# Kernel tuning notes

Hardware: AMD Instinct MI355X
Metric: run time of the kernel (lower is better)

Reference implementation:

```python
import jax, jax.numpy as jnp
import numpy as np

BATCH = 4096
DIM = 512
TEMP = 0.5

def setup_inputs() -> dict:
    key = jax.random.key(0)
    k1, k2 = jax.random.split(key)
    emb_i = jax.random.normal(k1, (BATCH, DIM), dtype=jnp.float32)
    emb_j = jax.random.normal(k2, (BATCH, DIM), dtype=jnp.float32)
    return {"emb_i": emb_i, "emb_j": emb_j}

def reference(emb_i, emb_j):
    n = emb_i.shape[0]
    # L2-normalize once (torch F.normalize uses eps=1e-12 clamp on norm)
    z_i = emb_i / jnp.maximum(jnp.linalg.norm(emb_i, axis=1, keepdims=True), 1e-12)
    z_j = emb_j / jnp.maximum(jnp.linalg.norm(emb_j, axis=1, keepdims=True), 1e-12)
    z = jnp.concatenate([z_i, z_j], axis=0)            # [2N, D]
    sim = jnp.einsum('nd,md->nm', z, z)                # cosine sim, single GEMM
    # positives: diag(sim, +N) and diag(sim, -N) == rowwise dot(z_i, z_j)
    pos_ij = jnp.sum(z_i * z_j, axis=1)                # [N]
    positives = jnp.concatenate([pos_ij, pos_ij], 0)   # [2N]
    exp_sim = jnp.exp(sim / TEMP)
    mask = 1.0 - jnp.eye(2 * n, dtype=sim.dtype)
    denom = jnp.sum(mask * exp_sim, axis=1)            # [2N]
    loss_partial = -(positives / TEMP - jnp.log(denom))
    return jnp.sum(loss_partial) / (2 * n)
```

## Files before the change

### kernel.cpp

```cpp
#include <hip/hip_runtime.h>
#include <hip/hip_bf16.h>

#define N_ROWS 4096
#define DIM 512
#define TWO_N 8192
#define NTILE 64
#define NTRI  (NTILE * (NTILE + 1) / 2)

typedef __bf16 bf16x8 __attribute__((ext_vector_type(8)));
typedef float  f32x4  __attribute__((ext_vector_type(4)));

__device__ inline unsigned short f2bf(float f) {
    unsigned int u = __float_as_uint(f);
    u += 0x7fffu + ((u >> 16) & 1u);
    return (unsigned short)(u >> 16);
}

__device__ inline void g2l16(const void* g, void* l) {
    __builtin_amdgcn_global_load_lds(
        (const __attribute__((address_space(1))) void*)g,
        (__attribute__((address_space(3))) void*)l,
        16, 0, 0);
}

__global__ void normalize_kernel(const float* __restrict__ ei,
                                 const float* __restrict__ ej,
                                 unsigned short* __restrict__ zb,
                                 float* __restrict__ pos,
                                 float* __restrict__ denom,
                                 float* __restrict__ out) {
    int r = blockIdx.x;
    int t = threadIdx.x;
    const float2 vi = ((const float2*)(ei + (size_t)r * DIM))[t];
    const float2 vj = ((const float2*)(ej + (size_t)r * DIM))[t];
    float si  = vi.x * vi.x + vi.y * vi.y;
    float sj  = vj.x * vj.x + vj.y * vj.y;
    float sij = vi.x * vj.x + vi.y * vj.y;

    for (int o = 32; o; o >>= 1) {
        si  += __shfl_down(si, o);
        sj  += __shfl_down(sj, o);
        sij += __shfl_down(sij, o);
    }
    __shared__ float red[3][4];
    int wave = t >> 6, lane = t & 63;
    if (lane == 0) { red[0][wave] = si; red[1][wave] = sj; red[2][wave] = sij; }
    __syncthreads();
    si  = red[0][0] + red[0][1] + red[0][2] + red[0][3];
    sj  = red[1][0] + red[1][1] + red[1][2] + red[1][3];
    sij = red[2][0] + red[2][1] + red[2][2] + red[2][3];

    float rni = 1.0f / fmaxf(sqrtf(si), 1e-12f);
    float rnj = 1.0f / fmaxf(sqrtf(sj), 1e-12f);
    if (t == 0) {
        pos[r] = sij * rni * rnj;
        denom[r] = 0.0f;
        denom[r + N_ROWS] = 0.0f;
        if (r == 0) out[0] = 0.0f;
    }
    ushort2 zi2 = make_ushort2(f2bf(vi.x * rni), f2bf(vi.y * rni));
    ushort2 zj2 = make_ushort2(f2bf(vj.x * rnj), f2bf(vj.y * rnj));
    ((ushort2*)(zb + (size_t)r * DIM))[t] = zi2;
    ((ushort2*)(zb + (size_t)(r + N_ROWS) * DIM))[t] = zj2;
}

__global__ __launch_bounds__(256, 4) void gemm_exp_kernel(
        const unsigned short* __restrict__ zb,
        float* __restrict__ denom) {
    const int t = blockIdx.x;
    int by = (int)(0.5f * (2.0f * NTILE + 1.0f -
              sqrtf((2.0f * NTILE + 1.0f) * (2.0f * NTILE + 1.0f) - 8.0f * t)));
    while ((by + 1) * NTILE - ((by + 1) * by) / 2 <= t) ++by;
    while (by * NTILE - (by * (by - 1)) / 2 > t) --by;
    const int bx = by + (t - (by * NTILE - (by * (by - 1)) / 2));

    const int rb = by * 128;
    const int cb = bx * 128;
    const bool diag = (rb == cb);

    const int tid  = threadIdx.x;
    const int wave = tid >> 6;
    const int lane = tid & 63;
    const int quad = lane >> 4;
    const int m    = lane & 15;
    const int wm   = (wave >> 1) * 64;
    const int wn   = (wave & 1) * 64;

    __shared__ __align__(16) unsigned short As[128 * 64];
    __shared__ __align__(16) unsigned short Bs[128 * 64];

    f32x4 acc[4][4];
    #pragma unroll
    for (int i = 0; i < 4; ++i)
        #pragma unroll
        for (int j = 0; j < 4; ++j)
            #pragma unroll
            for (int r = 0; r < 4; ++r) acc[i][j][r] = 0.0f;

    const int srow8 = lane >> 3;
    const int sk    = (((lane & 7) ^ srow8) * 8);

    for (int it = 0; it < DIM / 64; ++it) {
        if (it) __syncthreads();
        const int k0 = it * 64;
        #pragma unroll
        for (int cc = 0; cc < 4; ++cc) {
            int c   = 4 * wave + cc;
            int row = c * 8 + srow8;
            const unsigned short* ga = zb + (size_t)(rb + row) * DIM + k0 + sk;
            const unsigned short* gb = zb + (size_t)(cb + row) * DIM + k0 + sk;
            g2l16(ga, As + c * 512);
            g2l16(gb, Bs + c * 512);
        }
        __syncthreads();

        #pragma unroll
        for (int h = 0; h < 2; ++h) {
            bf16x8 af[4], bfr[4];
            const int sl = ((((h << 2) | quad) ^ (m & 7)) * 8);
            #pragma unroll
            for (int i = 0; i < 4; ++i)
                af[i] = *(const bf16x8*)(As + (wm + i * 16 + m) * 64 + sl);
            #pragma unroll
            for (int j = 0; j < 4; ++j)
                bfr[j] = *(const bf16x8*)(Bs + (wn + j * 16 + m) * 64 + sl);

            #pragma unroll
            for (int i = 0; i < 4; ++i)
                #pragma unroll
                for (int j = 0; j < 4; ++j)
                    acc[i][j] = __builtin_amdgcn_mfma_f32_16x16x32_bf16(
                        af[i], bfr[j], acc[i][j], 0, 0, 0);
        }
    }

    __syncthreads();

    float* rs = (float*)As;
    float* cs = rs + 128;
    if (tid < 128) { rs[tid] = 0.0f; cs[tid] = 0.0f; }
    __syncthreads();

    float colsum[4] = {0.0f, 0.0f, 0.0f, 0.0f};
    #pragma unroll
    for (int i = 0; i < 4; ++i) {
        #pragma unroll
        for (int r = 0; r < 4; ++r) {
            int lrow = wm + i * 16 + quad * 4 + r;
            int grow = rb + lrow;
            float s = 0.0f;
            #pragma unroll
            for (int j = 0; j < 4; ++j) {
                int gcol = cb + wn + j * 16 + m;
                float v  = __expf(2.0f * acc[i][j][r]);
                v = (grow == gcol) ? 0.0f : v;
                s += v;
                colsum[j] += v;
            }
            s += __shfl_xor(s, 1);
            s += __shfl_xor(s, 2);
            s += __shfl_xor(s, 4);
            s += __shfl_xor(s, 8);
            if (m == 0) atomicAdd(&rs[lrow], s);
        }
    }
    if (!diag) {
        #pragma unroll
        for (int j = 0; j < 4; ++j) {
            float s = colsum[j];
            s += __shfl_xor(s, 16);
            s += __shfl_xor(s, 32);
            if (quad == 0) atomicAdd(&cs[wn + j * 16 + m], s);
        }
    }
    __syncthreads();
    if (tid < 128) {
        atomicAdd(&denom[rb + tid], rs[tid]);
        if (!diag) atomicAdd(&denom[cb + tid], cs[tid]);
    }
}

__global__ void loss_kernel(const float* __restrict__ pos,
                            const float* __restrict__ denom,
                            float* __restrict__ out) {
    int r = blockIdx.x * 256 + threadIdx.x;
    float s = __logf(denom[r]) - 2.0f * pos[r & (N_ROWS - 1)];
    for (int o = 32; o; o >>= 1) s += __shfl_down(s, o);
    __shared__ float red[4];
    int t = threadIdx.x;
    if ((t & 63) == 0) red[t >> 6] = s;
    __syncthreads();
    if (t == 0)
        atomicAdd(out, (red[0] + red[1] + red[2] + red[3]) / (float)TWO_N);
}

extern "C" void kernel_launch(void* const* d_in, const int* in_sizes, int n_in,
                              void* d_out, int out_size, void* d_ws, size_t ws_size,
                              hipStream_t stream) {
    const float* ei = (const float*)d_in[0];
    const float* ej = (const float*)d_in[1];

    unsigned short* zb  = (unsigned short*)d_ws;
    float* pos   = (float*)((char*)d_ws + (size_t)TWO_N * DIM * sizeof(unsigned short));
    float* denom = pos + N_ROWS;
    float* out   = (float*)d_out;

    normalize_kernel<<<N_ROWS, 256, 0, stream>>>(ei, ej, zb, pos, denom, out);
    gemm_exp_kernel<<<NTRI, 256, 0, stream>>>(zb, denom);
    loss_kernel<<<TWO_N / 256, 256, 0, stream>>>(pos, denom, out);
}
```

Baseline: 122.1 us.

## Use 256x256 tiles with 8 waves and double-buffered LDS prefetch

```diff
diff --git a/kernel.cpp b/kernel.cpp
--- a/kernel.cpp
+++ b/kernel.cpp
@@ -4,8 +4,8 @@
 #define N_ROWS 4096
 #define DIM 512
 #define TWO_N 8192
-#define NTILE 64
-#define NTRI  (NTILE * (NTILE + 1) / 2)
+#define NT2   32
+#define NTRI2 (NT2 * (NT2 + 1) / 2)
 
 typedef __bf16 bf16x8 __attribute__((ext_vector_type(8)));
 typedef float  f32x4  __attribute__((ext_vector_type(4)));
@@ -64,18 +64,18 @@
     ((ushort2*)(zb + (size_t)(r + N_ROWS) * DIM))[t] = zj2;
 }
 
-__global__ __launch_bounds__(256, 4) void gemm_exp_kernel(
+__global__ __launch_bounds__(512, 2) void gemm_exp_kernel(
         const unsigned short* __restrict__ zb,
         float* __restrict__ denom) {
     const int t = blockIdx.x;
-    int by = (int)(0.5f * (2.0f * NTILE + 1.0f -
-              sqrtf((2.0f * NTILE + 1.0f) * (2.0f * NTILE + 1.0f) - 8.0f * t)));
-    while ((by + 1) * NTILE - ((by + 1) * by) / 2 <= t) ++by;
-    while (by * NTILE - (by * (by - 1)) / 2 > t) --by;
-    const int bx = by + (t - (by * NTILE - (by * (by - 1)) / 2));
-
-    const int rb = by * 128;
-    const int cb = bx * 128;
+    int by = (int)(0.5f * (2.0f * NT2 + 1.0f -
+              sqrtf((2.0f * NT2 + 1.0f) * (2.0f * NT2 + 1.0f) - 8.0f * t)));
+    while ((by + 1) * NT2 - ((by + 1) * by) / 2 <= t) ++by;
+    while (by * NT2 - (by * (by - 1)) / 2 > t) --by;
+    const int bx = by + (t - (by * NT2 - (by * (by - 1)) / 2));
+
+    const int rb = by * 256;
+    const int cb = bx * 256;
     const bool diag = (rb == cb);
 
     const int tid  = threadIdx.x;
@@ -83,15 +83,15 @@
     const int lane = tid & 63;
     const int quad = lane >> 4;
     const int m    = lane & 15;
-    const int wm   = (wave >> 1) * 64;
-    const int wn   = (wave & 1) * 64;
-
-    __shared__ __align__(16) unsigned short As[128 * 64];
-    __shared__ __align__(16) unsigned short Bs[128 * 64];
-
-    f32x4 acc[4][4];
+    const int wm   = (wave >> 2) * 128;
+    const int wn   = (wave & 3) * 64;
+
+    __shared__ __align__(16) unsigned short As[2][256 * 64];
+    __shared__ __align__(16) unsigned short Bs[2][256 * 64];
+
+    f32x4 acc[8][4];
     #pragma unroll
-    for (int i = 0; i < 4; ++i)
+    for (int i = 0; i < 8; ++i)
         #pragma unroll
         for (int j = 0; j < 4; ++j)
             #pragma unroll
@@ -100,50 +100,65 @@
     const int srow8 = lane >> 3;
     const int sk    = (((lane & 7) ^ srow8) * 8);
 
+    #pragma unroll
+    for (int cc = 0; cc < 4; ++cc) {
+        int c = 4 * wave + cc;
+        int row = c * 8 + srow8;
+        g2l16(zb + (size_t)(rb + row) * DIM + sk, &As[0][c * 512]);
+        g2l16(zb + (size_t)(cb + row) * DIM + sk, &Bs[0][c * 512]);
+    }
+    asm volatile("s_waitcnt vmcnt(0)" ::: "memory");
+    __builtin_amdgcn_s_barrier();
+
+    #pragma unroll 1
     for (int it = 0; it < DIM / 64; ++it) {
-        if (it) __syncthreads();
-        const int k0 = it * 64;
-        #pragma unroll
-        for (int cc = 0; cc < 4; ++cc) {
-            int c   = 4 * wave + cc;
-            int row = c * 8 + srow8;
-            const unsigned short* ga = zb + (size_t)(rb + row) * DIM + k0 + sk;
-            const unsigned short* gb = zb + (size_t)(cb + row) * DIM + k0 + sk;
-            g2l16(ga, As + c * 512);
-            g2l16(gb, Bs + c * 512);
-        }
-        __syncthreads();
+        const int cur = it & 1;
+        const int nxt = cur ^ 1;
+        const int k1  = (it + 1) * 64;
 
         #pragma unroll
         for (int h = 0; h < 2; ++h) {
-            bf16x8 af[4], bfr[4];
+            if (it < DIM / 64 - 1) {
+                #pragma unroll
+                for (int cc = 0; cc < 2; ++cc) {
+                    int c = 4 * wave + 2 * h + cc;
+                    int row = c * 8 + srow8;
+                    g2l16(zb + (size_t)(rb + row) * DIM + k1 + sk, &As[nxt][c * 512]);
+                    g2l16(zb + (size_t)(cb + row) * DIM + k1 + sk, &Bs[nxt][c * 512]);
+                }
+            }
+            bf16x8 af[8], bfr[4];
             const int sl = ((((h << 2) | quad) ^ (m & 7)) * 8);
             #pragma unroll
-            for (int i = 0; i < 4; ++i)
-                af[i] = *(const bf16x8*)(As + (wm + i * 16 + m) * 64 + sl);
+            for (int i = 0; i < 8; ++i)
+                af[i] = *(const bf16x8*)(&As[cur][(wm + i * 16 + m) * 64 + sl]);
             #pragma unroll
             for (int j = 0; j < 4; ++j)
-                bfr[j] = *(const bf16x8*)(Bs + (wn + j * 16 + m) * 64 + sl);
-
-            #pragma unroll
-            for (int i = 0; i < 4; ++i)
+                bfr[j] = *(const bf16x8*)(&Bs[cur][(wn + j * 16 + m) * 64 + sl]);
+
+            asm volatile("s_waitcnt lgkmcnt(0)" ::: "memory");
+            __builtin_amdgcn_sched_barrier(0);
+            __builtin_amdgcn_s_setprio(1);
+            #pragma unroll
+            for (int i = 0; i < 8; ++i)
                 #pragma unroll
                 for (int j = 0; j < 4; ++j)
                     acc[i][j] = __builtin_amdgcn_mfma_f32_16x16x32_bf16(
                         af[i], bfr[j], acc[i][j], 0, 0, 0);
+            __builtin_amdgcn_s_setprio(0);
         }
-    }
-
-    __syncthreads();
-
-    float* rs = (float*)As;
-    float* cs = rs + 128;
-    if (tid < 128) { rs[tid] = 0.0f; cs[tid] = 0.0f; }
+        asm volatile("s_waitcnt vmcnt(0)" ::: "memory");
+        __builtin_amdgcn_s_barrier();
+    }
+
+    float* rs = (float*)&As[0][0];
+    float* cs = rs + 256;
+    if (tid < 256) { rs[tid] = 0.0f; cs[tid] = 0.0f; }
     __syncthreads();
 
     float colsum[4] = {0.0f, 0.0f, 0.0f, 0.0f};
     #pragma unroll
-    for (int i = 0; i < 4; ++i) {
+    for (int i = 0; i < 8; ++i) {
         #pragma unroll
         for (int r = 0; r < 4; ++r) {
             int lrow = wm + i * 16 + quad * 4 + r;
@@ -174,7 +189,7 @@
         }
     }
     __syncthreads();
-    if (tid < 128) {
+    if (tid < 256) {
         atomicAdd(&denom[rb + tid], rs[tid]);
         if (!diag) atomicAdd(&denom[cb + tid], cs[tid]);
     }
@@ -206,6 +221,6 @@
     float* out   = (float*)d_out;
 
     normalize_kernel<<<N_ROWS, 256, 0, stream>>>(ei, ej, zb, pos, denom, out);
-    gemm_exp_kernel<<<NTRI, 256, 0, stream>>>(zb, denom);
+    gemm_exp_kernel<<<NTRI2, 512, 0, stream>>>(zb, denom);
     loss_kernel<<<TWO_N / 256, 256, 0, stream>>>(pos, denom, out);
 }
```

New measurement: 134.8 us. 1.1x slower.

## Fuse normalize, GEMM-exp and loss into one cooperative persistent kernel

Applied to the files above, without the earlier changes.

```diff
diff --git a/kernel.cpp b/kernel.cpp
--- a/kernel.cpp
+++ b/kernel.cpp
@@ -1,11 +1,15 @@
 #include <hip/hip_runtime.h>
 #include <hip/hip_bf16.h>
+#include <hip/hip_cooperative_groups.h>
+
+namespace cg = cooperative_groups;
 
 #define N_ROWS 4096
 #define DIM 512
 #define TWO_N 8192
 #define NTILE 64
 #define NTRI  (NTILE * (NTILE + 1) / 2)
+#define GRID  1024
 
 typedef __bf16 bf16x8 __attribute__((ext_vector_type(8)));
 typedef float  f32x4  __attribute__((ext_vector_type(4)));
@@ -23,45 +27,193 @@
         16, 0, 0);
 }
 
-__global__ void normalize_kernel(const float* __restrict__ ei,
-                                 const float* __restrict__ ej,
-                                 unsigned short* __restrict__ zb,
-                                 float* __restrict__ pos,
-                                 float* __restrict__ denom,
-                                 float* __restrict__ out) {
-    int r = blockIdx.x;
-    int t = threadIdx.x;
-    const float2 vi = ((const float2*)(ei + (size_t)r * DIM))[t];
-    const float2 vj = ((const float2*)(ej + (size_t)r * DIM))[t];
-    float si  = vi.x * vi.x + vi.y * vi.y;
-    float sj  = vj.x * vj.x + vj.y * vj.y;
-    float sij = vi.x * vj.x + vi.y * vj.y;
-
-    for (int o = 32; o; o >>= 1) {
-        si  += __shfl_down(si, o);
-        sj  += __shfl_down(sj, o);
-        sij += __shfl_down(sij, o);
-    }
-    __shared__ float red[3][4];
-    int wave = t >> 6, lane = t & 63;
-    if (lane == 0) { red[0][wave] = si; red[1][wave] = sj; red[2][wave] = sij; }
-    __syncthreads();
-    si  = red[0][0] + red[0][1] + red[0][2] + red[0][3];
-    sj  = red[1][0] + red[1][1] + red[1][2] + red[1][3];
-    sij = red[2][0] + red[2][1] + red[2][2] + red[2][3];
-
+__device__ inline void normalize_row(const float* __restrict__ ei,
+                                     const float* __restrict__ ej,
+                                     unsigned short* __restrict__ zb,
+                                     float* __restrict__ pos,
+                                     float* __restrict__ denom,
+                                     int r, int lane) {
+    const float4* pi = (const float4*)(ei + (size_t)r * DIM);
+    const float4* pj = (const float4*)(ej + (size_t)r * DIM);
+    float4 a0 = pi[lane * 2], a1 = pi[lane * 2 + 1];
+    float4 b0 = pj[lane * 2], b1 = pj[lane * 2 + 1];
+
+    float si  = a0.x*a0.x + a0.y*a0.y + a0.z*a0.z + a0.w*a0.w
+              + a1.x*a1.x + a1.y*a1.y + a1.z*a1.z + a1.w*a1.w;
+    float sj  = b0.x*b0.x + b0.y*b0.y + b0.z*b0.z + b0.w*b0.w
+              + b1.x*b1.x + b1.y*b1.y + b1.z*b1.z + b1.w*b1.w;
+    float sij = a0.x*b0.x + a0.y*b0.y + a0.z*b0.z + a0.w*b0.w
+              + a1.x*b1.x + a1.y*b1.y + a1.z*b1.z + a1.w*b1.w;
+
+    #pragma unroll
+    for (int o = 1; o < 64; o <<= 1) {
+        si  += __shfl_xor(si, o);
+        sj  += __shfl_xor(sj, o);
+        sij += __shfl_xor(sij, o);
+    }
     float rni = 1.0f / fmaxf(sqrtf(si), 1e-12f);
     float rnj = 1.0f / fmaxf(sqrtf(sj), 1e-12f);
-    if (t == 0) {
+    if (lane == 0) {
         pos[r] = sij * rni * rnj;
         denom[r] = 0.0f;
         denom[r + N_ROWS] = 0.0f;
-        if (r == 0) out[0] = 0.0f;
-    }
-    ushort2 zi2 = make_ushort2(f2bf(vi.x * rni), f2bf(vi.y * rni));
-    ushort2 zj2 = make_ushort2(f2bf(vj.x * rnj), f2bf(vj.y * rnj));
-    ((ushort2*)(zb + (size_t)r * DIM))[t] = zi2;
-    ((ushort2*)(zb + (size_t)(r + N_ROWS) * DIM))[t] = zj2;
+    }
+    union { unsigned short u[8]; uint4 v; } zi, zj;
+    zi.u[0] = f2bf(a0.x * rni); zi.u[1] = f2bf(a0.y * rni);
+    zi.u[2] = f2bf(a0.z * rni); zi.u[3] = f2bf(a0.w * rni);
+    zi.u[4] = f2bf(a1.x * rni); zi.u[5] = f2bf(a1.y * rni);
+    zi.u[6] = f2bf(a1.z * rni); zi.u[7] = f2bf(a1.w * rni);
+    zj.u[0] = f2bf(b0.x * rnj); zj.u[1] = f2bf(b0.y * rnj);
+    zj.u[2] = f2bf(b0.z * rnj); zj.u[3] = f2bf(b0.w * rnj);
+    zj.u[4] = f2bf(b1.x * rnj); zj.u[5] = f2bf(b1.y * rnj);
+    zj.u[6] = f2bf(b1.z * rnj); zj.u[7] = f2bf(b1.w * rnj);
+    ((uint4*)(zb + (size_t)r * DIM))[lane] = zi.v;
+    ((uint4*)(zb + (size_t)(r + N_ROWS) * DIM))[lane] = zj.v;
+}
+
+__global__ __launch_bounds__(256, 4) void mega_kernel(
+        const float* __restrict__ ei, const float* __restrict__ ej,
+        unsigned short* __restrict__ zb, float* __restrict__ pos,
+        float* __restrict__ denom, float* __restrict__ out) {
+    const int tid  = threadIdx.x;
+    const int wave = tid >> 6;
+    const int lane = tid & 63;
+
+    __shared__ __align__(16) unsigned short As[128 * 64];
+    __shared__ __align__(16) unsigned short Bs[128 * 64];
+
+    {
+        int r = blockIdx.x * 4 + wave;
+        normalize_row(ei, ej, zb, pos, denom, r, lane);
+        if (blockIdx.x == 0 && tid == 0) out[0] = 0.0f;
+    }
+    cg::this_grid().sync();
+
+    const int quad = lane >> 4;
+    const int m    = lane & 15;
+    const int wm   = (wave >> 1) * 64;
+    const int wn   = (wave & 1) * 64;
+    const int srow8 = lane >> 3;
+    const int sk    = (((lane & 7) ^ srow8) * 8);
+
+    for (int tix = blockIdx.x; tix < NTRI; tix += GRID) {
+        int by = (int)(0.5f * (2.0f * NTILE + 1.0f -
+                  sqrtf((2.0f * NTILE + 1.0f) * (2.0f * NTILE + 1.0f) - 8.0f * tix)));
+        while ((by + 1) * NTILE - ((by + 1) * by) / 2 <= tix) ++by;
+        while (by * NTILE - (by * (by - 1)) / 2 > tix) --by;
+        const int bx = by + (tix - (by * NTILE - (by * (by - 1)) / 2));
+        const int rb = by * 128;
+        const int cb = bx * 128;
+        const bool diag = (rb == cb);
+
+        f32x4 acc[4][4];
+        #pragma unroll
+        for (int i = 0; i < 4; ++i)
+            #pragma unroll
+            for (int j = 0; j < 4; ++j)
+                #pragma unroll
+                for (int r = 0; r < 4; ++r) acc[i][j][r] = 0.0f;
+
+        for (int it = 0; it < DIM / 64; ++it) {
+            __syncthreads();
+            const int k0 = it * 64;
+            #pragma unroll
+            for (int cc = 0; cc < 4; ++cc) {
+                int c   = 4 * wave + cc;
+                int row = c * 8 + srow8;
+                g2l16(zb + (size_t)(rb + row) * DIM + k0 + sk, As + c * 512);
+                g2l16(zb + (size_t)(cb + row) * DIM + k0 + sk, Bs + c * 512);
+            }
+            __syncthreads();
+
+            #pragma unroll
+            for (int h = 0; h < 2; ++h) {
+                bf16x8 af[4], bfr[4];
+                const int sl = ((((h << 2) | quad) ^ (m & 7)) * 8);
+                #pragma unroll
+                for (int i = 0; i < 4; ++i)
+                    af[i] = *(const bf16x8*)(As + (wm + i * 16 + m) * 64 + sl);
+                #pragma unroll
+                for (int j = 0; j < 4; ++j)
+                    bfr[j] = *(const bf16x8*)(Bs + (wn + j * 16 + m) * 64 + sl);
+
+                #pragma unroll
+                for (int i = 0; i < 4; ++i)
+                    #pragma unroll
+                    for (int j = 0; j < 4; ++j)
+                        acc[i][j] = __builtin_amdgcn_mfma_f32_16x16x32_bf16(
+                            af[i], bfr[j], acc[i][j], 0, 0, 0);
+            }
+        }
+        __syncthreads();
+
+        float* rs = (float*)As;
+        float* cs = rs + 128;
+        if (tid < 128) { rs[tid] = 0.0f; cs[tid] = 0.0f; }
+        __syncthreads();
+
+        float colsum[4] = {0.0f, 0.0f, 0.0f, 0.0f};
+        #pragma unroll
+        for (int i = 0; i < 4; ++i) {
+            #pragma unroll
+            for (int r = 0; r < 4; ++r) {
+                int lrow = wm + i * 16 + quad * 4 + r;
+                int grow = rb + lrow;
+                float s = 0.0f;
+                #pragma unroll
+                for (int j = 0; j < 4; ++j) {
+                    int gcol = cb + wn + j * 16 + m;
+                    float v  = __expf(2.0f * acc[i][j][r]);
+                    v = (grow == gcol) ? 0.0f : v;
+                    s += v;
+                    colsum[j] += v;
+                }
+                s += __shfl_xor(s, 1);
+                s += __shfl_xor(s, 2);
+                s += __shfl_xor(s, 4);
+                s += __shfl_xor(s, 8);
+                if (m == 0) atomicAdd(&rs[lrow], s);
+            }
+        }
+        if (!diag) {
+            #pragma unroll
+            for (int j = 0; j < 4; ++j) {
+                float s = colsum[j];
+                s += __shfl_xor(s, 16);
+                s += __shfl_xor(s, 32);
+                if (quad == 0) atomicAdd(&cs[wn + j * 16 + m], s);
+            }
+        }
+        __syncthreads();
+        if (tid < 128) {
+            atomicAdd(&denom[rb + tid], rs[tid]);
+            if (!diag) atomicAdd(&denom[cb + tid], cs[tid]);
+        }
+    }
+    cg::this_grid().sync();
+
+    if (blockIdx.x < TWO_N / 256) {
+        int r = blockIdx.x * 256 + tid;
+        float s = __logf(denom[r]) - 2.0f * pos[r & (N_ROWS - 1)];
+        for (int o = 32; o; o >>= 1) s += __shfl_down(s, o);
+        float* red = (float*)As;
+        if ((tid & 63) == 0) red[wave] = s;
+        __syncthreads();
+        if (tid == 0)
+            atomicAdd(out, (red[0] + red[1] + red[2] + red[3]) / (float)TWO_N);
+    }
+}
+
+__global__ void normalize_fast_kernel(const float* __restrict__ ei,
+                                      const float* __restrict__ ej,
+                                      unsigned short* __restrict__ zb,
+                                      float* __restrict__ pos,
+                                      float* __restrict__ denom,
+                                      float* __restrict__ out) {
+    int wave = threadIdx.x >> 6, lane = threadIdx.x & 63;
+    int r = blockIdx.x * 4 + wave;
+    normalize_row(ei, ej, zb, pos, denom, r, lane);
+    if (blockIdx.x == 0 && threadIdx.x == 0) out[0] = 0.0f;
 }
 
 __global__ __launch_bounds__(256, 4) void gemm_exp_kernel(
@@ -73,9 +225,7 @@
     while ((by + 1) * NTILE - ((by + 1) * by) / 2 <= t) ++by;
     while (by * NTILE - (by * (by - 1)) / 2 > t) --by;
     const int bx = by + (t - (by * NTILE - (by * (by - 1)) / 2));
-
-    const int rb = by * 128;
-    const int cb = bx * 128;
+    const int rb = by * 128, cb = bx * 128;
     const bool diag = (rb == cb);
 
     const int tid  = threadIdx.x;
@@ -107,10 +257,8 @@
         for (int cc = 0; cc < 4; ++cc) {
             int c   = 4 * wave + cc;
             int row = c * 8 + srow8;
-            const unsigned short* ga = zb + (size_t)(rb + row) * DIM + k0 + sk;
-            const unsigned short* gb = zb + (size_t)(cb + row) * DIM + k0 + sk;
-            g2l16(ga, As + c * 512);
-            g2l16(gb, Bs + c * 512);
+            g2l16(zb + (size_t)(rb + row) * DIM + k0 + sk, As + c * 512);
+            g2l16(zb + (size_t)(cb + row) * DIM + k0 + sk, Bs + c * 512);
         }
         __syncthreads();
 
@@ -124,7 +272,6 @@
             #pragma unroll
             for (int j = 0; j < 4; ++j)
                 bfr[j] = *(const bf16x8*)(Bs + (wn + j * 16 + m) * 64 + sl);
-
             #pragma unroll
             for (int i = 0; i < 4; ++i)
                 #pragma unroll
@@ -133,7 +280,6 @@
                         af[i], bfr[j], acc[i][j], 0, 0, 0);
         }
     }
-
     __syncthreads();
 
     float* rs = (float*)As;
@@ -205,7 +351,14 @@
     float* denom = pos + N_ROWS;
     float* out   = (float*)d_out;
 
-    normalize_kernel<<<N_ROWS, 256, 0, stream>>>(ei, ej, zb, pos, denom, out);
-    gemm_exp_kernel<<<NTRI, 256, 0, stream>>>(zb, denom);
-    loss_kernel<<<TWO_N / 256, 256, 0, stream>>>(pos, denom, out);
-}
+    void* kargs[] = {(void*)&ei, (void*)&ej, (void*)&zb,
+                     (void*)&pos, (void*)&denom, (void*)&out};
+    hipError_t err = hipLaunchCooperativeKernel(
+        (const void*)mega_kernel, dim3(GRID), dim3(256), kargs, 0, stream);
+    if (err != hipSuccess) {
+        (void)hipGetLastError();
+        normalize_fast_kernel<<<GRID, 256, 0, stream>>>(ei, ej, zb, pos, denom, out);
+        gemm_exp_kernel<<<NTRI, 256, 0, stream>>>(zb, denom);
+        loss_kernel<<<TWO_N / 256, 256, 0, stream>>>(pos, denom, out);
+    }
+}
```

Result: slower. 373.6 us (+206.1%).
